# Kernel tuning notes

Measured on AMD Instinct MI355X. Metric: run time of the kernel, lower is better.

Reference implementation:

```python
import jax, jax.numpy as jnp
import numpy as np

B, S, D = 4, 2048, 1024
H, HD = 16, 64
NDIM = 2                      # 2D RoPE (position_ids last dim)
PER_DIM = 2 * (HD // (2 * NDIM))   # 32 rotated dims per spatial axis
HALF = PER_DIM // 2                # 16
EPS = 1e-6


def setup_inputs() -> dict:
    key = jax.random.key(0)
    ks = jax.random.split(key, 10)
    sc = 0.02
    return {
        "hidden_states": jax.random.normal(ks[0], (B, S, D), jnp.float32),
        "cos": jax.random.uniform(ks[1], (B, S, HD), jnp.float32, -1.0, 1.0),
        "sin": jax.random.uniform(ks[2], (B, S, HD), jnp.float32, -1.0, 1.0),
        "position_ids": jax.random.randint(ks[3], (B, S, NDIM), 0, S, jnp.int64 if jax.config.x64_enabled else jnp.int32),
        # torch nn.Linear weights are [out_features, in_features]
        "wq": jax.random.normal(ks[4], (H * HD, D), jnp.float32) * sc,
        "wk": jax.random.normal(ks[5], (H * HD, D), jnp.float32) * sc,
        "wv": jax.random.normal(ks[6], (H * HD, D), jnp.float32) * sc,
        "wo": jax.random.normal(ks[7], (D, H * HD), jnp.float32) * sc,
        "q_scale": jnp.ones((HD,), jnp.float32),
        "k_scale": jnp.ones((HD,), jnp.float32),
    }


def _rms_norm(x, scale=None, eps=EPS):
    n = x * jax.lax.rsqrt(jnp.mean(x * x, axis=-1, keepdims=True) + eps)
    return n * scale if scale is not None else n


def _rotate_half(x):
    x1, x2 = x[..., :HALF], x[..., HALF:]
    return jnp.concatenate([-x2, x1], axis=-1)


def _rope2d(x, cos, sin):
    # x: [B,S,H,HD]; cos/sin: [B,S,HD]; rotate each NDIM chunk independently
    parts = []
    for k in range(NDIM):
        sl = slice(k * PER_DIM, (k + 1) * PER_DIM)
        xp = x[..., sl]
        cp = cos[:, :, None, sl]
        sp = sin[:, :, None, sl]
        parts.append(xp * cp + _rotate_half(xp) * sp)
    return jnp.concatenate(parts, axis=-1)


def reference(hidden_states, cos, sin, position_ids, wq, wk, wv, wo, q_scale, k_scale):
    b, s, _ = hidden_states.shape
    # QKV projections (clamp buffers default to +/-inf -> identity)
    q = (hidden_states @ wq.T).reshape(b, s, H, HD)
    k = (hidden_states @ wk.T).reshape(b, s, H, HD)
    v = (hidden_states @ wv.T).reshape(b, s, H, HD)
    # per-head RMSNorm (q/k with scale, v without)
    q = _rms_norm(q, q_scale)
    k = _rms_norm(k, k_scale)
    v = _rms_norm(v)
    # 2D RoPE on q and k
    q = _rope2d(q, cos, sin)
    k = _rope2d(k, cos, sin)
    # SDPA with scale=1.0 (as in the source), heads-major layout
    scores = jnp.einsum('bqhd,bkhd->bhqk', q, k)
    attn = jax.nn.softmax(scores, axis=-1)
    out = jnp.einsum('bhqk,bkhd->bqhd', attn, v).reshape(b, s, H * HD)
    return out @ wo.T
```

## Files before the change

### kernel.cpp

```cpp
#include <hip/hip_runtime.h>
#include <hip/hip_bf16.h>
#include <stdint.h>
#include <stddef.h>

#define B_ 4
#define S_ 2048
#define D_ 1024
#define H_ 16
#define HD_ 64
#define NTOK (B_*S_)
#define HDIM (H_*HD_)
#define LOG2E 1.44269504088896f

typedef __bf16 bf16_t;
typedef __bf16 bf16x4 __attribute__((ext_vector_type(4)));
typedef __bf16 bf16x8 __attribute__((ext_vector_type(8)));
typedef float floatx4 __attribute__((ext_vector_type(4)));

#define MFMA16(a,b,c)  __builtin_amdgcn_mfma_f32_16x16x32_bf16((a),(b),(c),0,0,0)

__device__ __forceinline__ void async_cp16(const bf16_t* g, bf16_t* l) {
    typedef __attribute__((address_space(1))) const unsigned int gu32;
    typedef __attribute__((address_space(3))) unsigned int lu32;
    __builtin_amdgcn_global_load_lds((gu32*)g, (lu32*)l, 16, 0, 0);
}

__device__ __forceinline__ bf16x8 cat44(bf16x4 a, bf16x4 b) {
    union { bf16x4 h[2]; bf16x8 v; } u;
    u.h[0] = a; u.h[1] = b;
    return u.v;
}

struct Cvt5 { const float* s[5]; bf16_t* d[5]; int n4[5]; };

__global__ __launch_bounds__(256) void cvt5(Cvt5 p) {
    const int z = blockIdx.y;
    const float4* __restrict__ src = (const float4*)p.s[z];
    bf16x4* __restrict__ dst = (bf16x4*)p.d[z];
    const int n4 = p.n4[z];
    for (int i = blockIdx.x * 256 + threadIdx.x; i < n4; i += gridDim.x * 256) {
        const float4 v = src[i];
        dst[i] = (bf16x4){(bf16_t)v.x, (bf16_t)v.y, (bf16_t)v.z, (bf16_t)v.w};
    }
}

struct GemmPtrs { const bf16_t* A[3]; const bf16_t* W[3]; void* C[3]; };

template<int MODE>
__global__ __launch_bounds__(256, 3) void gemm_nt(GemmPtrs p, int K) {
    __shared__ bf16_t lA0[128*32], lA1[128*32];
    __shared__ bf16_t lB0[128*32], lB1[128*32];
    const bf16_t* __restrict__ A = p.A[blockIdx.z];
    const bf16_t* __restrict__ W = p.W[blockIdx.z];
    const int m0 = blockIdx.y * 128;
    const int n0 = blockIdx.x * 128;
    const int t = threadIdx.x;
    const int lane = t & 63;
    const int wave = t >> 6;
    const int wm = wave >> 1;
    const int wn = wave & 1;
    const int l16 = lane & 15;
    const int quad = lane >> 4;

    const int srow0 = wave*32 + (lane >> 2);
    const int skc   = (lane & 3) * 8;

    floatx4 acc[4][4] = {};

    for (int k0 = 0; k0 < K; k0 += 64) {
        #pragma unroll
        for (int c = 0; c < 2; ++c) {
            const int row = srow0 + c*16;
            const size_t ao = (size_t)(m0+row)*K + k0 + skc;
            const size_t wo = (size_t)(n0+row)*K + k0 + skc;
            async_cp16(&A[ao],      &lA0[row*32 + skc]);
            async_cp16(&A[ao + 32], &lA1[row*32 + skc]);
            async_cp16(&W[wo],      &lB0[row*32 + skc]);
            async_cp16(&W[wo + 32], &lB1[row*32 + skc]);
        }
        __syncthreads();
        {
            bf16x8 af[4], bfr[4];
            #pragma unroll
            for (int i = 0; i < 4; ++i) {
                af[i]  = *(const bf16x8*)(&lA0[(wm*64 + i*16 + l16)*32 + quad*8]);
                bfr[i] = *(const bf16x8*)(&lB0[(wn*64 + i*16 + l16)*32 + quad*8]);
            }
            #pragma unroll
            for (int i = 0; i < 4; ++i)
                #pragma unroll
                for (int j = 0; j < 4; ++j)
                    acc[i][j] = MFMA16(af[i], bfr[j], acc[i][j]);
        }
        {
            bf16x8 af[4], bfr[4];
            #pragma unroll
            for (int i = 0; i < 4; ++i) {
                af[i]  = *(const bf16x8*)(&lA1[(wm*64 + i*16 + l16)*32 + quad*8]);
                bfr[i] = *(const bf16x8*)(&lB1[(wn*64 + i*16 + l16)*32 + quad*8]);
            }
            #pragma unroll
            for (int i = 0; i < 4; ++i)
                #pragma unroll
                for (int j = 0; j < 4; ++j)
                    acc[i][j] = MFMA16(af[i], bfr[j], acc[i][j]);
        }
        __syncthreads();
    }

    if (MODE == 1) {
        bf16_t* __restrict__ C = (bf16_t*)p.C[blockIdx.z];
        #pragma unroll
        for (int i = 0; i < 4; ++i) {
            const int mb = m0 + wm*64 + i*16 + quad*4;
            #pragma unroll
            for (int j = 0; j < 4; ++j) {
                const int n = n0 + wn*64 + j*16 + l16;
                const int h = n >> 6, d = n & 63;
                #pragma unroll
                for (int r = 0; r < 4; ++r) {
                    const int m = mb + r;
                    const int b = m >> 11, s = m & (S_-1);
                    C[(((size_t)b*H_ + h)*S_ + s)*HD_ + d] = (bf16_t)acc[i][j][r];
                }
            }
        }
    } else {
        float* __restrict__ C = (float*)p.C[blockIdx.z];
        #pragma unroll
        for (int i = 0; i < 4; ++i) {
            const int mb = m0 + wm*64 + i*16 + quad*4;
            #pragma unroll
            for (int j = 0; j < 4; ++j) {
                const int n = n0 + wn*64 + j*16 + l16;
                #pragma unroll
                for (int r = 0; r < 4; ++r)
                    C[(size_t)(mb + r)*HDIM + n] = acc[i][j][r];
            }
        }
    }
}

__global__ __launch_bounds__(256) void norm_rope(
    bf16_t* __restrict__ qb, bf16_t* __restrict__ kb,
    const bf16_t* __restrict__ vb, bf16_t* __restrict__ vt,
    const float* __restrict__ cs, const float* __restrict__ sn,
    const float* __restrict__ qscale, const float* __restrict__ kscale) {
    __shared__ bf16_t lv[64*65];
    const int bh = blockIdx.y;
    const int b  = bh >> 4;
    const int s0 = blockIdx.x * 64;
    const int t = threadIdx.x;
    const int wave = t >> 6;
    const int lane = t & 63;
    const float qsc = qscale[lane] * LOG2E;
    const float ksc = kscale[lane];
    const float sg = (lane & 16) ? 1.f : -1.f;

    for (int i = 0; i < 16; ++i) {
        const int s = s0 + wave*16 + i;
        const size_t addr = ((size_t)bh*S_ + s)*HD_ + lane;
        const float q = (float)qb[addr];
        const float k = (float)kb[addr];
        const float v = (float)vb[addr];
        float sq = q*q, sk = k*k, sv = v*v;
        #pragma unroll
        for (int m = 32; m; m >>= 1) {
            sq += __shfl_xor(sq, m);
            sk += __shfl_xor(sk, m);
            sv += __shfl_xor(sv, m);
        }
        float qv = q * rsqrtf(sq*(1.f/64.f) + 1e-6f) * qsc;
        float kv = k * rsqrtf(sk*(1.f/64.f) + 1e-6f) * ksc;
        const float vv = v * rsqrtf(sv*(1.f/64.f) + 1e-6f);
        const size_t ci = ((size_t)b*S_ + s)*HD_ + lane;
        const float c = cs[ci];
        const float sn_ = sn[ci];
        const float qo = __shfl_xor(qv, 16);
        const float ko = __shfl_xor(kv, 16);
        qv = qv*c + sg*qo*sn_;
        kv = kv*c + sg*ko*sn_;
        qb[addr] = (bf16_t)qv;
        kb[addr] = (bf16_t)kv;
        lv[(wave*16 + i)*65 + lane] = (bf16_t)vv;
    }
    __syncthreads();
    const int d = t >> 2;
    const int sc = (t & 3) * 16;
    bf16x8 o0, o1;
    #pragma unroll
    for (int e = 0; e < 8; ++e) {
        o0[e] = lv[(sc + e)*65 + d];
        o1[e] = lv[(sc + 8 + e)*65 + d];
    }
    bf16_t* dst = &vt[((size_t)bh*HD_ + d)*S_ + s0 + sc];
    *(bf16x8*)(dst)     = o0;
    *(bf16x8*)(dst + 8) = o1;
}

__global__ __launch_bounds__(512, 4) void flash_attn(
    const bf16_t* __restrict__ qn, const bf16_t* __restrict__ kn,
    const bf16_t* __restrict__ vt, bf16_t* __restrict__ attn_out) {
    __shared__ __align__(16) bf16_t sh[16384];

    const int bh = blockIdx.y;
    const int b  = bh >> 4;
    const int h  = bh & 15;
    const int q0 = blockIdx.x * 256;
    const int t = threadIdx.x;
    const int wave = t >> 6;
    const int lane = t & 63;
    const int l16 = lane & 15;
    const int quad = lane >> 4;
    const floatx4 finit = {-46.f, -46.f, -46.f, -46.f};

    const bf16_t* Q  = qn + (size_t)bh * S_ * HD_;
    const bf16_t* K  = kn + (size_t)bh * S_ * HD_;
    const bf16_t* Vt = vt + (size_t)bh * HD_ * S_;

    bf16x8 qf[2][2];
    #pragma unroll
    for (int rb = 0; rb < 2; ++rb) {
        const int qrow = q0 + wave*32 + rb*16 + l16;
        qf[rb][0] = *(const bf16x8*)(&Q[(size_t)qrow*HD_ + quad*8]);
        qf[rb][1] = *(const bf16x8*)(&Q[(size_t)qrow*HD_ + 32 + quad*8]);
    }

    floatx4 accO[2][4] = {};
    float accL[2] = {0.f, 0.f};

    const int sgrow = (wave & 3)*16 + l16;
    const int sgcol = (wave >> 2)*32 + quad*8;
    const int kwoff = (wave & 3)*1024 + (wave >> 2)*512 + lane*8;
    const int vU    = ((wave & 3)*2 + (wave >> 2))*64 + ((2*quad) & 3)*16 + l16;
    const int vwoff = vU*8 + (quad >> 1)*4;

    async_cp16(&K[(size_t)sgrow*HD_ + sgcol], &sh[kwoff]);
    {
        const bf16x8 v0 = *(const bf16x8*)(&Vt[(size_t)sgrow*S_ + sgcol]);
        union { bf16x8 v; bf16x4 hh[2]; } uv; uv.v = v0;
        *(bf16x4*)(&sh[8192 + vwoff])       = uv.hh[0];
        *(bf16x4*)(&sh[8192 + vwoff + 128]) = uv.hh[1];
    }

    bf16x8 vpre;
    for (int i = 0; i < S_/64; ++i) {
        __syncthreads();
        const bf16_t* lK = sh + (i & 1)*4096;
        const bf16_t* lV = sh + 8192 + (i & 1)*4096;
        const bool more = (i + 1 < S_/64);
        if (more) {
            const int ktn = (i + 1) * 64;
            async_cp16(&K[(size_t)(ktn + sgrow)*HD_ + sgcol],
                       &sh[((i+1) & 1)*4096 + kwoff]);
            vpre = *(const bf16x8*)(&Vt[(size_t)sgrow*S_ + ktn + sgcol]);
        }

        __builtin_amdgcn_s_setprio(1);
        bf16x4 pf[2][4];
        #pragma unroll
        for (int ct = 0; ct < 4; ++ct) {
            const bf16x8 kf0 = *(const bf16x8*)(&lK[ct*1024 + lane*8]);
            const bf16x8 kf1 = *(const bf16x8*)(&lK[ct*1024 + 512 + lane*8]);
            #pragma unroll
            for (int rb = 0; rb < 2; ++rb) {
                floatx4 s = MFMA16(kf0, qf[rb][0], finit);
                s = MFMA16(kf1, qf[rb][1], s);
                const float e0 = __builtin_amdgcn_exp2f(s[0]);
                const float e1 = __builtin_amdgcn_exp2f(s[1]);
                const float e2 = __builtin_amdgcn_exp2f(s[2]);
                const float e3 = __builtin_amdgcn_exp2f(s[3]);
                accL[rb] += (e0 + e1) + (e2 + e3);
                bf16x4 pb;
                pb[0] = (bf16_t)e0; pb[1] = (bf16_t)e1;
                pb[2] = (bf16_t)e2; pb[3] = (bf16_t)e3;
                pf[rb][ct] = pb;
            }
        }
        bf16x8 pb8[2][2];
        #pragma unroll
        for (int rb = 0; rb < 2; ++rb) {
            pb8[rb][0] = cat44(pf[rb][0], pf[rb][1]);
            pb8[rb][1] = cat44(pf[rb][2], pf[rb][3]);
        }
        #pragma unroll
        for (int dt = 0; dt < 4; ++dt) {
            #pragma unroll
            for (int c = 0; c < 2; ++c) {
                const bf16x8 vf = *(const bf16x8*)(&lV[(dt*2 + c)*512 + lane*8]);
                accO[0][dt] = MFMA16(vf, pb8[0][c], accO[0][dt]);
                accO[1][dt] = MFMA16(vf, pb8[1][c], accO[1][dt]);
            }
        }
        __builtin_amdgcn_s_setprio(0);

        if (more) {
            bf16_t* nV = sh + 8192 + ((i+1) & 1)*4096;
            union { bf16x8 v; bf16x4 hh[2]; } uv; uv.v = vpre;
            *(bf16x4*)(&nV[vwoff])       = uv.hh[0];
            *(bf16x4*)(&nV[vwoff + 128]) = uv.hh[1];
        }
    }

    __syncthreads();
    bf16_t* W = sh + wave * (16*72);
    #pragma unroll
    for (int rb = 0; rb < 2; ++rb) {
        float lr = accL[rb];
        lr += __shfl_xor(lr, 16);
        lr += __shfl_xor(lr, 32);
        const float inv = 1.f / lr;
        #pragma unroll
        for (int dt = 0; dt < 4; ++dt)
            #pragma unroll
            for (int r = 0; r < 4; ++r)
                W[l16*72 + dt*16 + quad*4 + r] = (bf16_t)(accO[rb][dt][r] * inv);
        #pragma unroll
        for (int half = 0; half < 2; ++half) {
            const int qr = half*8 + (lane >> 3);
            const bf16x8 o = *(const bf16x8*)(&W[qr*72 + (lane & 7)*8]);
            const int srw = q0 + wave*32 + rb*16 + qr;
            *(bf16x8*)(&attn_out[((size_t)b*S_ + srw)*HDIM + h*HD_ + (lane & 7)*8]) = o;
        }
    }
}

extern "C" void kernel_launch(void* const* d_in, const int* in_sizes, int n_in,
                              void* d_out, int out_size, void* d_ws, size_t ws_size,
                              hipStream_t stream) {
    (void)in_sizes; (void)n_in; (void)out_size; (void)ws_size;
    const float* X  = (const float*)d_in[0];
    const float* cs = (const float*)d_in[1];
    const float* sn = (const float*)d_in[2];
    const float* wq = (const float*)d_in[4];
    const float* wk = (const float*)d_in[5];
    const float* wv = (const float*)d_in[6];
    const float* wo = (const float*)d_in[7];
    const float* qs = (const float*)d_in[8];
    const float* ks = (const float*)d_in[9];
    float* out = (float*)d_out;

    const size_t PROJ = (size_t)NTOK * HDIM;
    const size_t WSZ  = (size_t)HDIM * D_;
    bf16_t* ws   = (bf16_t*)d_ws;
    bf16_t* Xb   = ws;
    bf16_t* wqb  = ws + PROJ;
    bf16_t* wkb  = wqb + WSZ;
    bf16_t* wvb  = wkb + WSZ;
    bf16_t* wob  = wvb + WSZ;
    bf16_t* qb   = wob + WSZ;
    bf16_t* kb   = qb + PROJ;
    bf16_t* vb   = kb + PROJ;
    bf16_t* vt   = Xb;
    bf16_t* attn = vb;

    Cvt5 cp;
    cp.s[0] = X;  cp.d[0] = Xb;  cp.n4[0] = (int)(PROJ/4);
    cp.s[1] = wq; cp.d[1] = wqb; cp.n4[1] = (int)(WSZ/4);
    cp.s[2] = wk; cp.d[2] = wkb; cp.n4[2] = (int)(WSZ/4);
    cp.s[3] = wv; cp.d[3] = wvb; cp.n4[3] = (int)(WSZ/4);
    cp.s[4] = wo; cp.d[4] = wob; cp.n4[4] = (int)(WSZ/4);
    cvt5<<<dim3(1024, 5), 256, 0, stream>>>(cp);

    GemmPtrs g1;
    g1.A[0] = Xb;  g1.A[1] = Xb;  g1.A[2] = Xb;
    g1.W[0] = wqb; g1.W[1] = wkb; g1.W[2] = wvb;
    g1.C[0] = qb;  g1.C[1] = kb;  g1.C[2] = vb;
    gemm_nt<1><<<dim3(HDIM/128, NTOK/128, 3), 256, 0, stream>>>(g1, D_);

    norm_rope<<<dim3(S_/64, B_*H_), 256, 0, stream>>>(qb, kb, vb, vt, cs, sn, qs, ks);

    flash_attn<<<dim3(S_/256, B_*H_), 512, 0, stream>>>(qb, kb, vt, attn);

    GemmPtrs g2;
    g2.A[0] = attn; g2.W[0] = wob; g2.C[0] = out;
    g2.A[1] = attn; g2.W[1] = wob; g2.C[1] = out;
    g2.A[2] = attn; g2.W[2] = wob; g2.C[2] = out;
    gemm_nt<2><<<dim3(HDIM/128, NTOK/128, 1), 256, 0, stream>>>(g2, HDIM);
}
```

Baseline: 297.0 us.

## Fuse per-head RMSNorm, 2D RoPE and V transpose into QKV GEMM epilogue

The QKV projection epilogue now computes each head's RMS over its 64 columns with cross-lane shuffles, then applies scale and RoPE to Q and K before storing bf16. For V it normalizes and writes the transposed layout through LDS. This removes the separate norm_rope kernel and its extra read and write pass over Q, K and V. In exchange the GEMM epilogue gets heavier (cos/sin loads, more registers) and the workspace buffer aliasing is reassigned.

```diff
diff --git a/kernel.cpp b/kernel.cpp
--- a/kernel.cpp
+++ b/kernel.cpp
@@ -44,12 +44,18 @@
     }
 }
 
-struct GemmPtrs { const bf16_t* A[3]; const bf16_t* W[3]; void* C[3]; };
+struct GemmPtrs {
+    const bf16_t* A[3]; const bf16_t* W[3]; void* C[3];
+    const float* cs; const float* sn; const float* qs; const float* ks;
+};
 
 template<int MODE>
 __global__ __launch_bounds__(256, 3) void gemm_nt(GemmPtrs p, int K) {
-    __shared__ bf16_t lA0[128*32], lA1[128*32];
-    __shared__ bf16_t lB0[128*32], lB1[128*32];
+    __shared__ bf16_t lds[4*4096];
+    bf16_t* lA0 = lds;
+    bf16_t* lA1 = lds + 4096;
+    bf16_t* lB0 = lds + 8192;
+    bf16_t* lB1 = lds + 12288;
     const bf16_t* __restrict__ A = p.A[blockIdx.z];
     const bf16_t* __restrict__ W = p.W[blockIdx.z];
     const int m0 = blockIdx.y * 128;
@@ -109,93 +115,95 @@
     }
 
     if (MODE == 1) {
-        bf16_t* __restrict__ C = (bf16_t*)p.C[blockIdx.z];
+        const int z = blockIdx.z;
+        const int h = blockIdx.x*2 + wn;
+        float inv[4][4];
+        #pragma unroll
+        for (int i = 0; i < 4; ++i) {
+            #pragma unroll
+            for (int r = 0; r < 4; ++r) {
+                float ssq = 0.f;
+                #pragma unroll
+                for (int j = 0; j < 4; ++j) ssq += acc[i][j][r]*acc[i][j][r];
+                ssq += __shfl_xor(ssq, 1);
+                ssq += __shfl_xor(ssq, 2);
+                ssq += __shfl_xor(ssq, 4);
+                ssq += __shfl_xor(ssq, 8);
+                inv[i][r] = rsqrtf(ssq*(1.f/64.f) + 1e-6f);
+            }
+        }
+        if (z < 2) {
+            bf16_t* __restrict__ C = (bf16_t*)p.C[z];
+            const float* __restrict__ scp = (z == 0) ? p.qs : p.ks;
+            const float scl = (z == 0) ? LOG2E : 1.f;
+            float qsl[4];
+            #pragma unroll
+            for (int j = 0; j < 4; ++j) qsl[j] = scp[j*16 + l16] * scl;
+            #pragma unroll
+            for (int i = 0; i < 4; ++i) {
+                #pragma unroll
+                for (int r = 0; r < 4; ++r) {
+                    const int m = m0 + wm*64 + i*16 + quad*4 + r;
+                    const int b = m >> 11, s = m & (S_-1);
+                    float nv[4];
+                    #pragma unroll
+                    for (int j = 0; j < 4; ++j) nv[j] = acc[i][j][r] * inv[i][r] * qsl[j];
+                    const float* cr = p.cs + ((size_t)b*S_ + s)*HD_ + l16;
+                    const float* sr = p.sn + ((size_t)b*S_ + s)*HD_ + l16;
+                    bf16_t* crow = &C[(((size_t)b*H_ + h)*S_ + s)*HD_ + l16];
+                    #pragma unroll
+                    for (int j = 0; j < 4; ++j) {
+                        const float sg = (j & 1) ? 1.f : -1.f;
+                        const float o = nv[j]*cr[j*16] + sg*nv[j^1]*sr[j*16];
+                        crow[j*16] = (bf16_t)o;
+                    }
+                }
+            }
+        } else {
+            bf16_t* __restrict__ Vt = (bf16_t*)p.C[2];
+            const int mbase = m0 + wm*64;
+            const int b = mbase >> 11;
+            const int sbase = mbase & (S_-1);
+            bf16_t* wl = lds + wave*2304;
+            #pragma unroll
+            for (int ps = 0; ps < 2; ++ps) {
+                #pragma unroll
+                for (int jj = 0; jj < 2; ++jj) {
+                    const int j = ps*2 + jj;
+                    const int dd = jj*16 + l16;
+                    #pragma unroll
+                    for (int i = 0; i < 4; ++i) {
+                        bf16x4 pk;
+                        #pragma unroll
+                        for (int r = 0; r < 4; ++r)
+                            pk[r] = (bf16_t)(acc[i][j][r] * inv[i][r]);
+                        *(bf16x4*)(&wl[dd*72 + i*16 + quad*4]) = pk;
+                    }
+                }
+                const int dloc = lane >> 1;
+                const int kh = (lane & 1) * 32;
+                bf16_t* dst = &Vt[((size_t)(b*H_ + h)*HD_ + ps*32 + dloc)*S_ + sbase + kh];
+                #pragma unroll
+                for (int c = 0; c < 4; ++c) {
+                    const bf16x8 vv = *(const bf16x8*)(&wl[dloc*72 + kh + c*8]);
+                    *(bf16x8*)(&dst[c*8]) = vv;
+                }
+            }
+        }
+    } else {
+        float* __restrict__ C = (float*)p.C[blockIdx.z];
         #pragma unroll
         for (int i = 0; i < 4; ++i) {
             const int mb = m0 + wm*64 + i*16 + quad*4;
             #pragma unroll
             for (int j = 0; j < 4; ++j) {
                 const int n = n0 + wn*64 + j*16 + l16;
-                const int h = n >> 6, d = n & 63;
-                #pragma unroll
-                for (int r = 0; r < 4; ++r) {
-                    const int m = mb + r;
-                    const int b = m >> 11, s = m & (S_-1);
-                    C[(((size_t)b*H_ + h)*S_ + s)*HD_ + d] = (bf16_t)acc[i][j][r];
-                }
-            }
-        }
-    } else {
-        float* __restrict__ C = (float*)p.C[blockIdx.z];
-        #pragma unroll
-        for (int i = 0; i < 4; ++i) {
-            const int mb = m0 + wm*64 + i*16 + quad*4;
-            #pragma unroll
-            for (int j = 0; j < 4; ++j) {
-                const int n = n0 + wn*64 + j*16 + l16;
                 #pragma unroll
                 for (int r = 0; r < 4; ++r)
                     C[(size_t)(mb + r)*HDIM + n] = acc[i][j][r];
             }
         }
     }
-}
-
-__global__ __launch_bounds__(256) void norm_rope(
-    bf16_t* __restrict__ qb, bf16_t* __restrict__ kb,
-    const bf16_t* __restrict__ vb, bf16_t* __restrict__ vt,
-    const float* __restrict__ cs, const float* __restrict__ sn,
-    const float* __restrict__ qscale, const float* __restrict__ kscale) {
-    __shared__ bf16_t lv[64*65];
-    const int bh = blockIdx.y;
-    const int b  = bh >> 4;
-    const int s0 = blockIdx.x * 64;
-    const int t = threadIdx.x;
-    const int wave = t >> 6;
-    const int lane = t & 63;
-    const float qsc = qscale[lane] * LOG2E;
-    const float ksc = kscale[lane];
-    const float sg = (lane & 16) ? 1.f : -1.f;
-
-    for (int i = 0; i < 16; ++i) {
-        const int s = s0 + wave*16 + i;
-        const size_t addr = ((size_t)bh*S_ + s)*HD_ + lane;
-        const float q = (float)qb[addr];
-        const float k = (float)kb[addr];
-        const float v = (float)vb[addr];
-        float sq = q*q, sk = k*k, sv = v*v;
-        #pragma unroll
-        for (int m = 32; m; m >>= 1) {
-            sq += __shfl_xor(sq, m);
-            sk += __shfl_xor(sk, m);
-            sv += __shfl_xor(sv, m);
-        }
-        float qv = q * rsqrtf(sq*(1.f/64.f) + 1e-6f) * qsc;
-        float kv = k * rsqrtf(sk*(1.f/64.f) + 1e-6f) * ksc;
-        const float vv = v * rsqrtf(sv*(1.f/64.f) + 1e-6f);
-        const size_t ci = ((size_t)b*S_ + s)*HD_ + lane;
-        const float c = cs[ci];
-        const float sn_ = sn[ci];
-        const float qo = __shfl_xor(qv, 16);
-        const float ko = __shfl_xor(kv, 16);
-        qv = qv*c + sg*qo*sn_;
-        kv = kv*c + sg*ko*sn_;
-        qb[addr] = (bf16_t)qv;
-        kb[addr] = (bf16_t)kv;
-        lv[(wave*16 + i)*65 + lane] = (bf16_t)vv;
-    }
-    __syncthreads();
-    const int d = t >> 2;
-    const int sc = (t & 3) * 16;
-    bf16x8 o0, o1;
-    #pragma unroll
-    for (int e = 0; e < 8; ++e) {
-        o0[e] = lv[(sc + e)*65 + d];
-        o1[e] = lv[(sc + 8 + e)*65 + d];
-    }
-    bf16_t* dst = &vt[((size_t)bh*HD_ + d)*S_ + s0 + sc];
-    *(bf16x8*)(dst)     = o0;
-    *(bf16x8*)(dst + 8) = o1;
 }
 
 __global__ __launch_bounds__(512, 4) void flash_attn(
@@ -351,8 +359,8 @@
     bf16_t* qb   = wob + WSZ;
     bf16_t* kb   = qb + PROJ;
     bf16_t* vb   = kb + PROJ;
-    bf16_t* vt   = Xb;
-    bf16_t* attn = vb;
+    bf16_t* vt   = vb;
+    bf16_t* attn = Xb;
 
     Cvt5 cp;
     cp.s[0] = X;  cp.d[0] = Xb;  cp.n4[0] = (int)(PROJ/4);
@@ -365,10 +373,9 @@
     GemmPtrs g1;
     g1.A[0] = Xb;  g1.A[1] = Xb;  g1.A[2] = Xb;
     g1.W[0] = wqb; g1.W[1] = wkb; g1.W[2] = wvb;
-    g1.C[0] = qb;  g1.C[1] = kb;  g1.C[2] = vb;
+    g1.C[0] = qb;  g1.C[1] = kb;  g1.C[2] = vt;
+    g1.cs = cs; g1.sn = sn; g1.qs = qs; g1.ks = ks;
     gemm_nt<1><<<dim3(HDIM/128, NTOK/128, 3), 256, 0, stream>>>(g1, D_);
-
-    norm_rope<<<dim3(S_/64, B_*H_), 256, 0, stream>>>(qb, kb, vb, vt, cs, sn, qs, ks);
 
     flash_attn<<<dim3(S_/256, B_*H_), 512, 0, stream>>>(qb, kb, vt, attn);
 
@@ -376,5 +383,6 @@
     g2.A[0] = attn; g2.W[0] = wob; g2.C[0] = out;
     g2.A[1] = attn; g2.W[1] = wob; g2.C[1] = out;
     g2.A[2] = attn; g2.W[2] = wob; g2.C[2] = out;
+    g2.cs = cs; g2.sn = sn; g2.qs = qs; g2.ks = ks;
     gemm_nt<2><<<dim3(HDIM/128, NTOK/128, 1), 256, 0, stream>>>(g2, HDIM);
 }
```

After: 279.9 us. 5.8% less time.
